# Optimization experiments

Measured on AMD Instinct MI355X. Metric: run time of the kernel, lower is better.

The kernel has to match this reference:

```python
import jax, jax.numpy as jnp
import numpy as np

B, T, E, H, TAG = 32, 1024, 512, 512, 2


def setup_inputs() -> dict:
    key = jax.random.key(0)
    ks = jax.random.split(key, 10)
    s = 1.0 / np.sqrt(H)
    u = lambda k, shape: jax.random.uniform(k, shape, jnp.float32, -s, s)
    xs = jax.random.normal(ks[0], (B, T, E), jnp.float32)
    lengths = jnp.sort(jax.random.randint(ks[1], (B,), 1, T + 1))[::-1]  # pack_padded wants descending
    domains = jnp.ones((B,), jnp.int32)  # single-domain path -> plain model + classification
    return dict(
        xs=xs, lengths=lengths, domains=domains,
        w_ih_f=u(ks[2], (4 * H, E)), w_hh_f=u(ks[3], (4 * H, H)), b_f=u(ks[4], (4 * H,)),
        w_ih_b=u(ks[5], (4 * H, E)), w_hh_b=u(ks[6], (4 * H, H)), b_b=u(ks[7], (4 * H,)),
        w_cls=u(ks[8], (TAG, 2 * H)), b_cls=u(ks[9], (TAG,)),
    )


def _run_lstm(xw, mask, w_hh):
    # xw: [T,B,4H] precomputed x @ W_ih^T + b ; mask: [T,B,1] valid positions
    Hd = w_hh.shape[1]
    Bn = xw.shape[1]

    def step(carry, inp):
        h, c = carry
        xw_t, m = inp
        g = xw_t + h @ w_hh.T                         # [B,4H], torch gate order i,f,g,o
        i, f, gg, o = jnp.split(g, 4, axis=-1)
        c_new = jax.nn.sigmoid(f) * c + jax.nn.sigmoid(i) * jnp.tanh(gg)
        h_new = jax.nn.sigmoid(o) * jnp.tanh(c_new)
        h = jnp.where(m, h_new, h)                    # packed seq: state frozen past length
        c = jnp.where(m, c_new, c)
        return (h, c), h_new * m                      # padded output is zero past length

    init = (jnp.zeros((Bn, Hd), xw.dtype), jnp.zeros((Bn, Hd), xw.dtype))
    _, outs = jax.lax.scan(step, init, (xw, mask))
    return outs  # [T,B,H]


def reference(xs, lengths, domains, w_ih_f, w_hh_f, b_f, w_ih_b, w_hh_b, b_b, w_cls, b_cls):
    Bn, Tn, _ = xs.shape
    t = jnp.arange(Tn)
    mask = (t[:, None] < lengths[None, :])[:, :, None]            # [T,B,1]
    # forward direction
    xw_f = jnp.einsum('bte,ge->tbg', xs, w_ih_f) + b_f
    out_f = _run_lstm(xw_f, mask, w_hh_f)                          # [T,B,H]
    # backward direction: reverse the valid prefix of each sequence
    idx = jnp.where(t[None, :] < lengths[:, None],
                    lengths[:, None] - 1 - t[None, :], t[None, :])  # [B,T]
    xs_rev = jnp.take_along_axis(xs, idx[:, :, None], axis=1)
    xw_b = jnp.einsum('bte,ge->tbg', xs_rev, w_ih_b) + b_b
    out_b_rev = _run_lstm(xw_b, mask, w_hh_b)                      # [T,B,H]
    out_b = jnp.take_along_axis(out_b_rev.transpose(1, 0, 2), idx[:, :, None], axis=1)
    out_b = out_b * mask.transpose(1, 0, 2)                        # zero padded positions
    h = jnp.concatenate([out_f.transpose(1, 0, 2), out_b], axis=-1)  # [B,T,2H]
    logits = h @ w_cls.T + b_cls                                   # [B,T,TAG]
    return jax.nn.softmax(logits, axis=2)
```

## Files before the change

### kernel.cpp

```cpp
#include <hip/hip_runtime.h>
#include <math.h>

#define B_N 32
#define T_N 1024
#define E_N 512
#define H_N 512
#define G4_N 2048

typedef __attribute__((ext_vector_type(8))) short short8;
typedef __attribute__((ext_vector_type(4))) float f32x4;
typedef __attribute__((ext_vector_type(4))) unsigned int uint32x4;
typedef unsigned long long ull;

__device__ __forceinline__ unsigned short f2bfu(float f) {
  unsigned int x = __builtin_bit_cast(unsigned int, f);
  x += 0x7fffu + ((x >> 16) & 1u);
  return (unsigned short)(x >> 16);
}
__device__ __forceinline__ float bfu2f(unsigned short u) {
  return __builtin_bit_cast(float, ((unsigned int)u) << 16);
}
__device__ __forceinline__ float sigmf(float x) { return 1.0f / (1.0f + expf(-x)); }

__device__ __forceinline__ void load64_mall(const unsigned short* p,
                                            uint32x4& a, uint32x4& b,
                                            uint32x4& c, uint32x4& d) {
  asm volatile("global_load_dwordx4 %0, %4, off sc0 sc1\n\t"
               "global_load_dwordx4 %1, %4, off offset:16 sc0 sc1\n\t"
               "global_load_dwordx4 %2, %4, off offset:32 sc0 sc1\n\t"
               "global_load_dwordx4 %3, %4, off offset:48 sc0 sc1\n\t"
               "s_waitcnt vmcnt(0)"
               : "=&v"(a), "=&v"(b), "=&v"(c), "=&v"(d)
               : "v"(p) : "memory");
}
__device__ __forceinline__ void store32_mall(unsigned int* p, unsigned int v) {
  asm volatile("global_store_dword %0, %1, off sc0 sc1" :: "v"(p), "v"(v) : "memory");
}

__global__ __launch_bounds__(256) void xw_gemm_kernel(
    const float* __restrict__ xs, const int* __restrict__ lengths,
    const float* __restrict__ w_ih_f, const float* __restrict__ b_f,
    const float* __restrict__ w_ih_b, const float* __restrict__ b_b,
    unsigned short* __restrict__ xw, int t0, int Tseg)
{
  __shared__ unsigned short As[64][80];
  __shared__ unsigned short Bs[64][80];
  const int g0 = blockIdx.x * 64;
  const int n0 = blockIdx.y * 64;
  const int dir = blockIdx.z;
  const float* __restrict__ W = dir ? w_ih_b : w_ih_f;
  const float* __restrict__ bias = dir ? b_b : b_f;
  const int tid = threadIdx.x;
  const int w = tid >> 6, lane = tid & 63;
  const int wr = w >> 1, wc = w & 1;

  const int sr = tid >> 2;
  const int sq = tid & 3;
  const int nrow = n0 + sr;
  const int bb = nrow & 31;
  const int tt = t0 + (nrow >> 5);
  const int Lb = lengths[bb];
  const int src_t = (dir != 0 && tt < Lb) ? (Lb - 1 - tt) : tt;
  const float* __restrict__ xrow = xs + ((size_t)bb * T_N + src_t) * E_N;
  const float* __restrict__ arow = W + (size_t)(g0 + sr) * E_N;

  f32x4 acc[2][2] = {};

  for (int k0 = 0; k0 < E_N; k0 += 64) {
    float4 av[4], bv[4];
#pragma unroll
    for (int i = 0; i < 4; ++i) {
      av[i] = *(const float4*)&arow[k0 + sq * 16 + i * 4];
      bv[i] = *(const float4*)&xrow[k0 + sq * 16 + i * 4];
    }
    __syncthreads();
#pragma unroll
    for (int i = 0; i < 4; ++i) {
      ushort4 a4, b4;
      a4.x = f2bfu(av[i].x); a4.y = f2bfu(av[i].y); a4.z = f2bfu(av[i].z); a4.w = f2bfu(av[i].w);
      b4.x = f2bfu(bv[i].x); b4.y = f2bfu(bv[i].y); b4.z = f2bfu(bv[i].z); b4.w = f2bfu(bv[i].w);
      *(ushort4*)&As[sr][sq * 16 + i * 4] = a4;
      *(ushort4*)&Bs[sr][sq * 16 + i * 4] = b4;
    }
    __syncthreads();
#pragma unroll
    for (int kk = 0; kk < 2; ++kk) {
      const int ko = kk * 32 + ((lane >> 4) << 3);
      short8 bf0 = *(const short8*)&Bs[wc * 32 + (lane & 15)][ko];
      short8 bf1 = *(const short8*)&Bs[wc * 32 + 16 + (lane & 15)][ko];
      short8 af0 = *(const short8*)&As[wr * 32 + (lane & 15)][ko];
      short8 af1 = *(const short8*)&As[wr * 32 + 16 + (lane & 15)][ko];
      acc[0][0] = __builtin_amdgcn_mfma_f32_16x16x32_bf16(af0, bf0, acc[0][0], 0, 0, 0);
      acc[0][1] = __builtin_amdgcn_mfma_f32_16x16x32_bf16(af0, bf1, acc[0][1], 0, 0, 0);
      acc[1][0] = __builtin_amdgcn_mfma_f32_16x16x32_bf16(af1, bf0, acc[1][0], 0, 0, 0);
      acc[1][1] = __builtin_amdgcn_mfma_f32_16x16x32_bf16(af1, bf1, acc[1][1], 0, 0, 0);
    }
  }

#pragma unroll
  for (int mt = 0; mt < 2; ++mt)
#pragma unroll
    for (int nt = 0; nt < 2; ++nt)
#pragma unroll
      for (int j = 0; j < 4; ++j) {
        const int m = g0 + wr * 32 + mt * 16 + ((lane >> 4) << 2) + j;
        const int n = n0 + wc * 32 + nt * 16 + (lane & 15);
        const int tl = n >> 5, b = n & 31;
        const float v = acc[mt][nt][j] + bias[m];
        xw[(((size_t)dir * Tseg + tl) * G4_N + m) * B_N + b] = f2bfu(v);
      }
}

__global__ __launch_bounds__(512, 1) void rec_kernel(
    const unsigned short* __restrict__ xw,
    const float* __restrict__ w_hh_f, const float* __restrict__ w_hh_b,
    const float* __restrict__ w_cls, const int* __restrict__ lengths,
    unsigned short* __restrict__ hx,
    unsigned int* __restrict__ flg,
    float* __restrict__ c_buf,
    float* __restrict__ lpart,
    int t0, int Tseg)
{
  __shared__ unsigned short Ah[32][520];
  __shared__ float gate_p[8][32][17];
  __shared__ float lp[16][33][2];

  const int tid = threadIdx.x;
  const int wg = blockIdx.x;
  const int dir = wg & 1;
  const int cg = wg >> 1;
  const int colbase = cg * 16;
  const float* __restrict__ w_hh = dir ? w_hh_b : w_hh_f;
  const int w = tid >> 6, lane = tid & 63;
  const int q = w >> 1, kh = w & 1;

  short8 wfrag[8];
  {
    const int grow = q * 512 + colbase + (lane & 15);
    const int kb = (lane >> 4) << 3;
    const float* __restrict__ wr_ = &w_hh[(size_t)grow * H_N + kh * 256];
#pragma unroll
    for (int ks = 0; ks < 8; ++ks) {
      const float4 f0 = *(const float4*)&wr_[ks * 32 + kb];
      const float4 f1 = *(const float4*)&wr_[ks * 32 + kb + 4];
      short8 v;
      v[0] = (short)f2bfu(f0.x); v[1] = (short)f2bfu(f0.y);
      v[2] = (short)f2bfu(f0.z); v[3] = (short)f2bfu(f0.w);
      v[4] = (short)f2bfu(f1.x); v[5] = (short)f2bfu(f1.y);
      v[6] = (short)f2bfu(f1.z); v[7] = (short)f2bfu(f1.w);
      wfrag[ks] = v;
    }
  }

  const int b = tid >> 4;
  const int cl = tid & 15;
  const int col = colbase + cl;
  const int Lb = lengths[b];
  const int Lb_r = lengths[tid & 31];
  float cc = c_buf[((size_t)dir * B_N + b) * H_N + col];
  const float wc0 = w_cls[dir * H_N + col];
  const float wc1 = w_cls[2 * H_N + dir * H_N + col];

  float hh = bfu2f(hx[((size_t)dir * 2 + (t0 & 1)) * 16384 + ((size_t)cg * 32 + b) * 16 + cl]);

  float* __restrict__ lslice = lpart + (size_t)wg * B_N * T_N * 2;
  unsigned int* __restrict__ myflag = flg + dir * 512 + cg * 16;
  unsigned int* __restrict__ pollflag = flg + dir * 512 + (tid >> 4) * 16;

  unsigned short xv[4];
  {
    const unsigned short* __restrict__ xb =
        &xw[((size_t)(dir * Tseg) * G4_N + colbase + cl) * B_N + b];
#pragma unroll
    for (int q2 = 0; q2 < 4; ++q2) xv[q2] = xb[(size_t)q2 * 512 * B_N];
  }

  for (int ts = 0; ts < Tseg; ++ts) {
    const int t = t0 + ts;

    if (ts > 0 && tid < 64) {
      const int br = tid & 31, tau = tid >> 5;
      const int tp = t - 1;
      if (tp < Lb_r) {
        float s = 0.f;
#pragma unroll
        for (int k = 0; k < 16; ++k) s += lp[k][br][tau];
        const int tpos = dir ? (Lb_r - 1 - tp) : tp;
        lslice[((size_t)br * T_N + tpos) * 2 + tau] = s;
      }
    }

    {
      const unsigned int want = (unsigned int)t;
      while (__hip_atomic_load(pollflag, __ATOMIC_RELAXED, __HIP_MEMORY_SCOPE_AGENT) < want) {}
    }
    {
      const unsigned short* hsrc =
          hx + ((size_t)dir * 2 + (t & 1)) * 16384 + (size_t)tid * 32;
      uint32x4 va, vb, vc, vd;
      load64_mall(hsrc, va, vb, vc, vd);
      const int b0 = (tid & 15) * 2, cg16 = (tid >> 4) * 16;
      *(uint32x4*)&Ah[b0][cg16] = va;
      *(uint32x4*)&Ah[b0][cg16 + 8] = vb;
      *(uint32x4*)&Ah[b0 + 1][cg16] = vc;
      *(uint32x4*)&Ah[b0 + 1][cg16 + 8] = vd;
    }
    __syncthreads();

    {
      f32x4 acc0 = {0.f, 0.f, 0.f, 0.f}, acc1 = {0.f, 0.f, 0.f, 0.f};
      const int kb = (lane >> 4) << 3;
#pragma unroll
      for (int ks = 0; ks < 8; ++ks) {
        const int kk = kh * 256 + (ks << 5) + kb;
        short8 a0 = *(const short8*)&Ah[(lane & 15)][kk];
        short8 a1 = *(const short8*)&Ah[16 + (lane & 15)][kk];
        acc0 = __builtin_amdgcn_mfma_f32_16x16x32_bf16(a0, wfrag[ks], acc0, 0, 0, 0);
        acc1 = __builtin_amdgcn_mfma_f32_16x16x32_bf16(a1, wfrag[ks], acc1, 0, 0, 0);
      }
      const int crow = (lane >> 4) << 2;
      const int ccol = lane & 15;
#pragma unroll
      for (int j = 0; j < 4; ++j) {
        gate_p[w][crow + j][ccol] = acc0[j];
        gate_p[w][16 + crow + j][ccol] = acc1[j];
      }
    }
    __syncthreads();

    const bool valid = (t < Lb);
    float hn;
    {
      const float gi = gate_p[0][b][cl] + gate_p[1][b][cl] + bfu2f(xv[0]);
      const float gf = gate_p[2][b][cl] + gate_p[3][b][cl] + bfu2f(xv[1]);
      const float gg = gate_p[4][b][cl] + gate_p[5][b][cl] + bfu2f(xv[2]);
      const float go = gate_p[6][b][cl] + gate_p[7][b][cl] + bfu2f(xv[3]);
      const float cn = sigmf(gf) * cc + sigmf(gi) * tanhf(gg);
      hn = sigmf(go) * tanhf(cn);
      if (valid) { cc = cn; hh = hn; }
    }

    {
      const float hhp = __shfl_xor(hh, 1);
      if ((cl & 1) == 0) {
        const unsigned int pv =
            (unsigned int)f2bfu(hh) | ((unsigned int)f2bfu(hhp) << 16);
        store32_mall((unsigned int*)(hx + ((size_t)dir * 2 + ((t + 1) & 1)) * 16384 +
                                     ((size_t)cg * 32 + b) * 16 + cl),
                     pv);
      }
    }
    lp[cl][b][0] = valid ? hn * wc0 : 0.f;
    lp[cl][b][1] = valid ? hn * wc1 : 0.f;

    __syncthreads();
    if (tid == 0)
      __hip_atomic_store(myflag, (unsigned int)(t + 1),
                         __ATOMIC_RELAXED, __HIP_MEMORY_SCOPE_AGENT);

    if (ts + 1 < Tseg) {
      const unsigned short* __restrict__ xb =
          &xw[((size_t)(dir * Tseg + ts + 1) * G4_N + colbase + cl) * B_N + b];
#pragma unroll
      for (int q2 = 0; q2 < 4; ++q2) xv[q2] = xb[(size_t)q2 * 512 * B_N];
    }
  }

  if (tid < 64) {
    const int br = tid & 31, tau = tid >> 5;
    const int tp = t0 + Tseg - 1;
    if (tp < Lb_r) {
      float s = 0.f;
#pragma unroll
      for (int k = 0; k < 16; ++k) s += lp[k][br][tau];
      const int tpos = dir ? (Lb_r - 1 - tp) : tp;
      lslice[((size_t)br * T_N + tpos) * 2 + tau] = s;
    }
  }

  c_buf[((size_t)dir * B_N + b) * H_N + col] = cc;
}

__global__ void init_kernel(ull* __restrict__ hx64, float* __restrict__ c_buf,
                            unsigned int* __restrict__ flg)
{
  const int i = blockIdx.x * 256 + threadIdx.x;
  if (i < 16384) hx64[i] = 0ull;
  if (i < 2 * B_N * H_N) c_buf[i] = 0.f;
  if (i < 1024) flg[i] = 0u;
}

__global__ void reduce_softmax_kernel(const float* __restrict__ lpart,
                                      const float* __restrict__ b_cls,
                                      float* __restrict__ out)
{
  const int i = blockIdx.x * 256 + threadIdx.x;
  if (i >= B_N * T_N) return;
  float s0 = b_cls[0], s1 = b_cls[1];
  const float* __restrict__ p = lpart + (size_t)i * 2;
#pragma unroll 8
  for (int wg = 0; wg < 64; ++wg) {
    s0 += p[(size_t)wg * B_N * T_N * 2];
    s1 += p[(size_t)wg * B_N * T_N * 2 + 1];
  }
  const float m = fmaxf(s0, s1);
  const float e0 = expf(s0 - m), e1 = expf(s1 - m);
  const float inv = 1.f / (e0 + e1);
  out[2 * i] = e0 * inv;
  out[2 * i + 1] = e1 * inv;
}

extern "C" void kernel_launch(void* const* d_in, const int* in_sizes, int n_in,
                              void* d_out, int out_size, void* d_ws, size_t ws_size,
                              hipStream_t stream)
{
  const float* xs      = (const float*)d_in[0];
  const int*   lengths = (const int*)d_in[1];
  const float* w_ih_f  = (const float*)d_in[3];
  const float* w_hh_f  = (const float*)d_in[4];
  const float* b_f     = (const float*)d_in[5];
  const float* w_ih_b  = (const float*)d_in[6];
  const float* w_hh_b  = (const float*)d_in[7];
  const float* b_b     = (const float*)d_in[8];
  const float* w_cls   = (const float*)d_in[9];
  const float* b_cls   = (const float*)d_in[10];
  float* out = (float*)d_out;

  auto alignup = [](size_t v) { return (v + 255) & ~(size_t)255; };
  const size_t hx_b    = alignup((size_t)2 * 2 * 32 * 32 * 16 * 2);
  const size_t flg_b   = alignup((size_t)1024 * 4);
  const size_t cbuf_b  = alignup((size_t)2 * B_N * H_N * 4);
  const size_t lpart_b = alignup((size_t)64 * B_N * T_N * 2 * 4);
  const size_t fixed = hx_b + flg_b + cbuf_b + lpart_b + 1024;

  int nseg = 1;
  while (nseg < 64) {
    const size_t xwb = alignup((size_t)2 * (T_N / nseg) * G4_N * B_N * 2);
    if (xwb + fixed <= ws_size) break;
    nseg <<= 1;
  }
  const int Tseg = T_N / nseg;
  const size_t xw_b = alignup((size_t)2 * Tseg * G4_N * B_N * 2);

  char* p = (char*)d_ws;
  unsigned short* xw = (unsigned short*)p;  p += xw_b;
  unsigned short* hx = (unsigned short*)p;  p += hx_b;
  unsigned int* flg = (unsigned int*)p;     p += flg_b;
  float* c_buf = (float*)p;                 p += cbuf_b;
  float* lpart = (float*)p;                 p += lpart_b;

  hipMemsetAsync(lpart, 0, lpart_b, stream);
  init_kernel<<<256, 256, 0, stream>>>((ull*)hx, c_buf, flg);

  for (int s = 0; s < nseg; ++s) {
    const int t0 = s * Tseg;
    dim3 g(G4_N / 64, (Tseg * B_N) / 64, 2);
    xw_gemm_kernel<<<g, 256, 0, stream>>>(xs, lengths, w_ih_f, b_f, w_ih_b, b_b, xw, t0, Tseg);
    rec_kernel<<<64, 512, 0, stream>>>(xw, w_hh_f, w_hh_b, w_cls, lengths,
                                       hx, flg, c_buf, lpart, t0, Tseg);
  }

  reduce_softmax_kernel<<<128, 256, 0, stream>>>(lpart, b_cls, out);
}
```

Measured before the change: 4.330 ms.

## Interleave both LSTM directions per workgroup with speculative prefetch of hidden state

```diff
diff --git a/kernel.cpp b/kernel.cpp
--- a/kernel.cpp
+++ b/kernel.cpp
@@ -30,6 +30,16 @@
                "global_load_dwordx4 %2, %4, off offset:32 sc0 sc1\n\t"
                "global_load_dwordx4 %3, %4, off offset:48 sc0 sc1\n\t"
                "s_waitcnt vmcnt(0)"
+               : "=&v"(a), "=&v"(b), "=&v"(c), "=&v"(d)
+               : "v"(p) : "memory");
+}
+__device__ __forceinline__ void load64_mall_nowait(const unsigned short* p,
+                                                   uint32x4& a, uint32x4& b,
+                                                   uint32x4& c, uint32x4& d) {
+  asm volatile("global_load_dwordx4 %0, %4, off sc0 sc1\n\t"
+               "global_load_dwordx4 %1, %4, off offset:16 sc0 sc1\n\t"
+               "global_load_dwordx4 %2, %4, off offset:32 sc0 sc1\n\t"
+               "global_load_dwordx4 %3, %4, off offset:48 sc0 sc1"
                : "=&v"(a), "=&v"(b), "=&v"(c), "=&v"(d)
                : "v"(p) : "memory");
 }
@@ -123,22 +133,26 @@
 {
   __shared__ unsigned short Ah[32][520];
   __shared__ float gate_p[8][32][17];
-  __shared__ float lp[16][33][2];
+  __shared__ float lp[2][16][33][2];
 
   const int tid = threadIdx.x;
-  const int wg = blockIdx.x;
-  const int dir = wg & 1;
-  const int cg = wg >> 1;
+  const int cg = blockIdx.x;
   const int colbase = cg * 16;
-  const float* __restrict__ w_hh = dir ? w_hh_b : w_hh_f;
   const int w = tid >> 6, lane = tid & 63;
   const int q = w >> 1, kh = w & 1;
-
-  short8 wfrag[8];
-  {
+  const int b = tid >> 4;
+  const int cl = tid & 15;
+  const int col = colbase + cl;
+  const int Lb = lengths[b];
+  const int Lb_r = lengths[tid & 31];
+
+  short8 wfrag[2][8];
+#pragma unroll
+  for (int d = 0; d < 2; ++d) {
+    const float* __restrict__ whh = d ? w_hh_b : w_hh_f;
     const int grow = q * 512 + colbase + (lane & 15);
     const int kb = (lane >> 4) << 3;
-    const float* __restrict__ wr_ = &w_hh[(size_t)grow * H_N + kh * 256];
+    const float* __restrict__ wr_ = &whh[(size_t)grow * H_N + kh * 256];
 #pragma unroll
     for (int ks = 0; ks < 8; ++ks) {
       const float4 f0 = *(const float4*)&wr_[ks * 32 + kb];
@@ -148,137 +162,164 @@
       v[2] = (short)f2bfu(f0.z); v[3] = (short)f2bfu(f0.w);
       v[4] = (short)f2bfu(f1.x); v[5] = (short)f2bfu(f1.y);
       v[6] = (short)f2bfu(f1.z); v[7] = (short)f2bfu(f1.w);
-      wfrag[ks] = v;
-    }
-  }
-
-  const int b = tid >> 4;
-  const int cl = tid & 15;
-  const int col = colbase + cl;
-  const int Lb = lengths[b];
-  const int Lb_r = lengths[tid & 31];
-  float cc = c_buf[((size_t)dir * B_N + b) * H_N + col];
-  const float wc0 = w_cls[dir * H_N + col];
-  const float wc1 = w_cls[2 * H_N + dir * H_N + col];
-
-  float hh = bfu2f(hx[((size_t)dir * 2 + (t0 & 1)) * 16384 + ((size_t)cg * 32 + b) * 16 + cl]);
-
-  float* __restrict__ lslice = lpart + (size_t)wg * B_N * T_N * 2;
-  unsigned int* __restrict__ myflag = flg + dir * 512 + cg * 16;
-  unsigned int* __restrict__ pollflag = flg + dir * 512 + (tid >> 4) * 16;
-
-  unsigned short xv[4];
-  {
+      wfrag[d][ks] = v;
+    }
+  }
+
+  float cc[2], hh[2], wc0[2], wc1[2];
+#pragma unroll
+  for (int d = 0; d < 2; ++d) {
+    cc[d] = c_buf[((size_t)d * B_N + b) * H_N + col];
+    hh[d] = bfu2f(hx[((size_t)d * 2 + (t0 & 1)) * 16384 + ((size_t)cg * 32 + b) * 16 + cl]);
+    wc0[d] = w_cls[d * H_N + col];
+    wc1[d] = w_cls[2 * H_N + d * H_N + col];
+  }
+
+  unsigned short xv[2][4];
+#pragma unroll
+  for (int d = 0; d < 2; ++d) {
     const unsigned short* __restrict__ xb =
-        &xw[((size_t)(dir * Tseg) * G4_N + colbase + cl) * B_N + b];
-#pragma unroll
-    for (int q2 = 0; q2 < 4; ++q2) xv[q2] = xb[(size_t)q2 * 512 * B_N];
-  }
+        &xw[((size_t)(d * Tseg) * G4_N + colbase + cl) * B_N + b];
+#pragma unroll
+    for (int q2 = 0; q2 < 4; ++q2) xv[d][q2] = xb[(size_t)q2 * 512 * B_N];
+  }
+
+  uint32x4 sp0, sp1, sp2, sp3;
+  bool spok[2] = {false, false};
+
+  const int myfw = (tid & 15) >> 1;
+  const int b0 = (tid & 15) * 2, cg16 = (tid >> 4) * 16;
 
   for (int ts = 0; ts < Tseg; ++ts) {
     const int t = t0 + ts;
 
-    if (ts > 0 && tid < 64) {
+#pragma unroll
+    for (int d = 0; d < 2; ++d) {
+      const int e = d ^ 1;
+      const int te = t + d;
+
+      if (spok[d]) {
+        asm volatile("s_waitcnt vmcnt(0)" ::: "memory");
+        __builtin_amdgcn_sched_barrier(0);
+        *(uint32x4*)&Ah[b0][cg16] = sp0;
+        *(uint32x4*)&Ah[b0][cg16 + 8] = sp1;
+        *(uint32x4*)&Ah[b0 + 1][cg16] = sp2;
+        *(uint32x4*)&Ah[b0 + 1][cg16 + 8] = sp3;
+      } else {
+        unsigned int* pf = flg + ((size_t)d * 32 + (tid >> 4)) * 8 + myfw;
+        while (__hip_atomic_load(pf, __ATOMIC_RELAXED, __HIP_MEMORY_SCOPE_AGENT) < (unsigned int)t) {}
+        uint32x4 va, vb, vc, vd;
+        load64_mall(hx + ((size_t)d * 2 + (t & 1)) * 16384 + (size_t)tid * 32, va, vb, vc, vd);
+        *(uint32x4*)&Ah[b0][cg16] = va;
+        *(uint32x4*)&Ah[b0][cg16 + 8] = vb;
+        *(uint32x4*)&Ah[b0 + 1][cg16] = vc;
+        *(uint32x4*)&Ah[b0 + 1][cg16 + 8] = vd;
+      }
+      unsigned int fve = __hip_atomic_load(
+          flg + ((size_t)e * 32 + (tid >> 4)) * 8 + myfw,
+          __ATOMIC_RELAXED, __HIP_MEMORY_SCOPE_AGENT);
+
+      __syncthreads();
+
+      if (ts > 0 && tid < 64) {
+        const int br = tid & 31, tau = tid >> 5;
+        const int tp = t - 1;
+        if (tp < Lb_r) {
+          float s = 0.f;
+#pragma unroll
+          for (int k = 0; k < 16; ++k) s += lp[d][k][br][tau];
+          const int tpos = d ? (Lb_r - 1 - tp) : tp;
+          lpart[((size_t)(cg * 2 + d) * B_N + br) * T_N * 2 + (size_t)tpos * 2 + tau] = s;
+        }
+      }
+      unsigned short xvn[4];
+      if (ts + 1 < Tseg) {
+        const unsigned short* __restrict__ xb =
+            &xw[((size_t)(d * Tseg + ts + 1) * G4_N + colbase + cl) * B_N + b];
+#pragma unroll
+        for (int q2 = 0; q2 < 4; ++q2) xvn[q2] = xb[(size_t)q2 * 512 * B_N];
+      }
+
+      {
+        f32x4 acc0 = {0.f, 0.f, 0.f, 0.f}, acc1 = {0.f, 0.f, 0.f, 0.f};
+        const int kb = (lane >> 4) << 3;
+#pragma unroll
+        for (int ks = 0; ks < 8; ++ks) {
+          const int kk = kh * 256 + (ks << 5) + kb;
+          short8 a0 = *(const short8*)&Ah[(lane & 15)][kk];
+          short8 a1 = *(const short8*)&Ah[16 + (lane & 15)][kk];
+          acc0 = __builtin_amdgcn_mfma_f32_16x16x32_bf16(a0, wfrag[d][ks], acc0, 0, 0, 0);
+          acc1 = __builtin_amdgcn_mfma_f32_16x16x32_bf16(a1, wfrag[d][ks], acc1, 0, 0, 0);
+        }
+        const int crow = (lane >> 4) << 2;
+        const int ccol = lane & 15;
+#pragma unroll
+        for (int j = 0; j < 4; ++j) {
+          gate_p[w][crow + j][ccol] = acc0[j];
+          gate_p[w][16 + crow + j][ccol] = acc1[j];
+        }
+      }
+      __syncthreads();
+
+      {
+        const bool in_seg = (d == 0) || (ts + 1 < Tseg);
+        const bool ok = in_seg && __all(fve >= (unsigned int)te);
+        if (ok) {
+          load64_mall_nowait(hx + ((size_t)e * 2 + (te & 1)) * 16384 + (size_t)tid * 32,
+                             sp0, sp1, sp2, sp3);
+        }
+        spok[e] = ok;
+      }
+
+      const bool valid = (t < Lb);
+      float hn;
+      {
+        const float gi = gate_p[0][b][cl] + gate_p[1][b][cl] + bfu2f(xv[d][0]);
+        const float gf = gate_p[2][b][cl] + gate_p[3][b][cl] + bfu2f(xv[d][1]);
+        const float gg = gate_p[4][b][cl] + gate_p[5][b][cl] + bfu2f(xv[d][2]);
+        const float go = gate_p[6][b][cl] + gate_p[7][b][cl] + bfu2f(xv[d][3]);
+        const float cn = sigmf(gf) * cc[d] + sigmf(gi) * tanhf(gg);
+        hn = sigmf(go) * tanhf(cn);
+        if (valid) { cc[d] = cn; hh[d] = hn; }
+      }
+      lp[d][cl][b][0] = valid ? hn * wc0[d] : 0.f;
+      lp[d][cl][b][1] = valid ? hn * wc1[d] : 0.f;
+#pragma unroll
+      for (int q2 = 0; q2 < 4; ++q2) xv[d][q2] = xvn[q2];
+
+      {
+        const float hhp = __shfl_xor(hh[d], 1);
+        if ((cl & 1) == 0) {
+          const unsigned int pv =
+              (unsigned int)f2bfu(hh[d]) | ((unsigned int)f2bfu(hhp) << 16);
+          store32_mall((unsigned int*)(hx + ((size_t)d * 2 + ((t + 1) & 1)) * 16384 +
+                                       ((size_t)cg * 32 + b) * 16 + cl),
+                       pv);
+        }
+      }
+
+      asm volatile("s_waitcnt vmcnt(0)" ::: "memory");
+      __builtin_amdgcn_sched_barrier(0);
+      if (lane == 0)
+        store32_mall(flg + ((size_t)d * 32 + cg) * 8 + w, (unsigned int)(t + 1));
+    }
+  }
+
+#pragma unroll
+  for (int d = 0; d < 2; ++d) {
+    if (tid < 64) {
       const int br = tid & 31, tau = tid >> 5;
-      const int tp = t - 1;
+      const int tp = t0 + Tseg - 1;
       if (tp < Lb_r) {
         float s = 0.f;
 #pragma unroll
-        for (int k = 0; k < 16; ++k) s += lp[k][br][tau];
-        const int tpos = dir ? (Lb_r - 1 - tp) : tp;
-        lslice[((size_t)br * T_N + tpos) * 2 + tau] = s;
-      }
-    }
-
-    {
-      const unsigned int want = (unsigned int)t;
-      while (__hip_atomic_load(pollflag, __ATOMIC_RELAXED, __HIP_MEMORY_SCOPE_AGENT) < want) {}
-    }
-    {
-      const unsigned short* hsrc =
-          hx + ((size_t)dir * 2 + (t & 1)) * 16384 + (size_t)tid * 32;
-      uint32x4 va, vb, vc, vd;
-      load64_mall(hsrc, va, vb, vc, vd);
-      const int b0 = (tid & 15) * 2, cg16 = (tid >> 4) * 16;
-      *(uint32x4*)&Ah[b0][cg16] = va;
-      *(uint32x4*)&Ah[b0][cg16 + 8] = vb;
-      *(uint32x4*)&Ah[b0 + 1][cg16] = vc;
-      *(uint32x4*)&Ah[b0 + 1][cg16 + 8] = vd;
-    }
-    __syncthreads();
-
-    {
-      f32x4 acc0 = {0.f, 0.f, 0.f, 0.f}, acc1 = {0.f, 0.f, 0.f, 0.f};
-      const int kb = (lane >> 4) << 3;
-#pragma unroll
-      for (int ks = 0; ks < 8; ++ks) {
-        const int kk = kh * 256 + (ks << 5) + kb;
-        short8 a0 = *(const short8*)&Ah[(lane & 15)][kk];
-        short8 a1 = *(const short8*)&Ah[16 + (lane & 15)][kk];
-        acc0 = __builtin_amdgcn_mfma_f32_16x16x32_bf16(a0, wfrag[ks], acc0, 0, 0, 0);
-        acc1 = __builtin_amdgcn_mfma_f32_16x16x32_bf16(a1, wfrag[ks], acc1, 0, 0, 0);
-      }
-      const int crow = (lane >> 4) << 2;
-      const int ccol = lane & 15;
-#pragma unroll
-      for (int j = 0; j < 4; ++j) {
-        gate_p[w][crow + j][ccol] = acc0[j];
-        gate_p[w][16 + crow + j][ccol] = acc1[j];
-      }
-    }
-    __syncthreads();
-
-    const bool valid = (t < Lb);
-    float hn;
-    {
-      const float gi = gate_p[0][b][cl] + gate_p[1][b][cl] + bfu2f(xv[0]);
-      const float gf = gate_p[2][b][cl] + gate_p[3][b][cl] + bfu2f(xv[1]);
-      const float gg = gate_p[4][b][cl] + gate_p[5][b][cl] + bfu2f(xv[2]);
-      const float go = gate_p[6][b][cl] + gate_p[7][b][cl] + bfu2f(xv[3]);
-      const float cn = sigmf(gf) * cc + sigmf(gi) * tanhf(gg);
-      hn = sigmf(go) * tanhf(cn);
-      if (valid) { cc = cn; hh = hn; }
-    }
-
-    {
-      const float hhp = __shfl_xor(hh, 1);
-      if ((cl & 1) == 0) {
-        const unsigned int pv =
-            (unsigned int)f2bfu(hh) | ((unsigned int)f2bfu(hhp) << 16);
-        store32_mall((unsigned int*)(hx + ((size_t)dir * 2 + ((t + 1) & 1)) * 16384 +
-                                     ((size_t)cg * 32 + b) * 16 + cl),
-                     pv);
-      }
-    }
-    lp[cl][b][0] = valid ? hn * wc0 : 0.f;
-    lp[cl][b][1] = valid ? hn * wc1 : 0.f;
-
-    __syncthreads();
-    if (tid == 0)
-      __hip_atomic_store(myflag, (unsigned int)(t + 1),
-                         __ATOMIC_RELAXED, __HIP_MEMORY_SCOPE_AGENT);
-
-    if (ts + 1 < Tseg) {
-      const unsigned short* __restrict__ xb =
-          &xw[((size_t)(dir * Tseg + ts + 1) * G4_N + colbase + cl) * B_N + b];
-#pragma unroll
-      for (int q2 = 0; q2 < 4; ++q2) xv[q2] = xb[(size_t)q2 * 512 * B_N];
-    }
-  }
-
-  if (tid < 64) {
-    const int br = tid & 31, tau = tid >> 5;
-    const int tp = t0 + Tseg - 1;
-    if (tp < Lb_r) {
-      float s = 0.f;
-#pragma unroll
-      for (int k = 0; k < 16; ++k) s += lp[k][br][tau];
-      const int tpos = dir ? (Lb_r - 1 - tp) : tp;
-      lslice[((size_t)br * T_N + tpos) * 2 + tau] = s;
-    }
-  }
-
-  c_buf[((size_t)dir * B_N + b) * H_N + col] = cc;
+        for (int k = 0; k < 16; ++k) s += lp[d][k][br][tau];
+        const int tpos = d ? (Lb_r - 1 - tp) : tp;
+        lpart[((size_t)(cg * 2 + d) * B_N + br) * T_N * 2 + (size_t)tpos * 2 + tau] = s;
+      }
+    }
+    c_buf[((size_t)d * B_N + b) * H_N + col] = cc[d];
+  }
 }
 
 __global__ void init_kernel(ull* __restrict__ hx64, float* __restrict__ c_buf,
@@ -287,7 +328,7 @@
   const int i = blockIdx.x * 256 + threadIdx.x;
   if (i < 16384) hx64[i] = 0ull;
   if (i < 2 * B_N * H_N) c_buf[i] = 0.f;
-  if (i < 1024) flg[i] = 0u;
+  if (i < 512) flg[i] = 0u;
 }
 
 __global__ void reduce_softmax_kernel(const float* __restrict__ lpart,
@@ -328,7 +369,7 @@
 
   auto alignup = [](size_t v) { return (v + 255) & ~(size_t)255; };
   const size_t hx_b    = alignup((size_t)2 * 2 * 32 * 32 * 16 * 2);
-  const size_t flg_b   = alignup((size_t)1024 * 4);
+  const size_t flg_b   = alignup((size_t)512 * 4);
   const size_t cbuf_b  = alignup((size_t)2 * B_N * H_N * 4);
   const size_t lpart_b = alignup((size_t)64 * B_N * T_N * 2 * 4);
   const size_t fixed = hx_b + flg_b + cbuf_b + lpart_b + 1024;
@@ -356,7 +397,7 @@
     const int t0 = s * Tseg;
     dim3 g(G4_N / 64, (Tseg * B_N) / 64, 2);
     xw_gemm_kernel<<<g, 256, 0, stream>>>(xs, lengths, w_ih_f, b_f, w_ih_b, b_b, xw, t0, Tseg);
-    rec_kernel<<<64, 512, 0, stream>>>(xw, w_hh_f, w_hh_b, w_cls, lengths,
+    rec_kernel<<<32, 512, 0, stream>>>(xw, w_hh_f, w_hh_b, w_cls, lengths,
                                        hx, flg, c_buf, lpart, t0, Tseg);
   }
 
```

Result: slower. 7.855 ms (+81.4%).

## Use per-wave completion flags and pipelined polling in recurrent LSTM loop

Applied to the files above, without the earlier changes.

```diff
diff --git a/kernel.cpp b/kernel.cpp
--- a/kernel.cpp
+++ b/kernel.cpp
@@ -37,6 +37,23 @@
   asm volatile("global_store_dword %0, %1, off sc0 sc1" :: "v"(p), "v"(v) : "memory");
 }
 
+__device__ __forceinline__ void poll_flag2(const unsigned int* pf, unsigned int want) {
+  unsigned int fa, fb;
+  asm volatile("global_load_dword %0, %2, off sc0 sc1\n\t"
+               "global_load_dword %1, %2, off sc0 sc1"
+               : "=&v"(fa), "=&v"(fb) : "v"(pf) : "memory");
+  for (;;) {
+    asm volatile("s_waitcnt vmcnt(1)" ::: "memory");
+    __builtin_amdgcn_sched_barrier(0);
+    if (fa >= want) break;
+    asm volatile("global_load_dword %0, %1, off sc0 sc1" : "=&v"(fa) : "v"(pf) : "memory");
+    asm volatile("s_waitcnt vmcnt(1)" ::: "memory");
+    __builtin_amdgcn_sched_barrier(0);
+    if (fb >= want) break;
+    asm volatile("global_load_dword %0, %1, off sc0 sc1" : "=&v"(fb) : "v"(pf) : "memory");
+  }
+}
+
 __global__ __launch_bounds__(256) void xw_gemm_kernel(
     const float* __restrict__ xs, const int* __restrict__ lengths,
     const float* __restrict__ w_ih_f, const float* __restrict__ b_f,
@@ -164,8 +181,9 @@
   float hh = bfu2f(hx[((size_t)dir * 2 + (t0 & 1)) * 16384 + ((size_t)cg * 32 + b) * 16 + cl]);
 
   float* __restrict__ lslice = lpart + (size_t)wg * B_N * T_N * 2;
-  unsigned int* __restrict__ myflag = flg + dir * 512 + cg * 16;
-  unsigned int* __restrict__ pollflag = flg + dir * 512 + (tid >> 4) * 16;
+  unsigned int* __restrict__ myflag = flg + ((size_t)dir * 32 + cg) * 8 + w;
+  const unsigned int* __restrict__ pollflag =
+      flg + ((size_t)dir * 32 + (tid >> 4)) * 8 + ((tid & 15) >> 1);
 
   unsigned short xv[4];
   {
@@ -175,8 +193,22 @@
     for (int q2 = 0; q2 < 4; ++q2) xv[q2] = xb[(size_t)q2 * 512 * B_N];
   }
 
+  const int b0 = (tid & 15) * 2, cg16 = (tid >> 4) * 16;
+
   for (int ts = 0; ts < Tseg; ++ts) {
     const int t = t0 + ts;
+
+    poll_flag2(pollflag, (unsigned int)t);
+    {
+      uint32x4 va, vb, vc, vd;
+      load64_mall(hx + ((size_t)dir * 2 + (t & 1)) * 16384 + (size_t)tid * 32,
+                  va, vb, vc, vd);
+      *(uint32x4*)&Ah[b0][cg16] = va;
+      *(uint32x4*)&Ah[b0][cg16 + 8] = vb;
+      *(uint32x4*)&Ah[b0 + 1][cg16] = vc;
+      *(uint32x4*)&Ah[b0 + 1][cg16 + 8] = vd;
+    }
+    __syncthreads();
 
     if (ts > 0 && tid < 64) {
       const int br = tid & 31, tau = tid >> 5;
@@ -189,23 +221,6 @@
         lslice[((size_t)br * T_N + tpos) * 2 + tau] = s;
       }
     }
-
-    {
-      const unsigned int want = (unsigned int)t;
-      while (__hip_atomic_load(pollflag, __ATOMIC_RELAXED, __HIP_MEMORY_SCOPE_AGENT) < want) {}
-    }
-    {
-      const unsigned short* hsrc =
-          hx + ((size_t)dir * 2 + (t & 1)) * 16384 + (size_t)tid * 32;
-      uint32x4 va, vb, vc, vd;
-      load64_mall(hsrc, va, vb, vc, vd);
-      const int b0 = (tid & 15) * 2, cg16 = (tid >> 4) * 16;
-      *(uint32x4*)&Ah[b0][cg16] = va;
-      *(uint32x4*)&Ah[b0][cg16 + 8] = vb;
-      *(uint32x4*)&Ah[b0 + 1][cg16] = vc;
-      *(uint32x4*)&Ah[b0 + 1][cg16 + 8] = vd;
-    }
-    __syncthreads();
 
     {
       f32x4 acc0 = {0.f, 0.f, 0.f, 0.f}, acc1 = {0.f, 0.f, 0.f, 0.f};
@@ -253,10 +268,10 @@
     lp[cl][b][0] = valid ? hn * wc0 : 0.f;
     lp[cl][b][1] = valid ? hn * wc1 : 0.f;
 
-    __syncthreads();
-    if (tid == 0)
-      __hip_atomic_store(myflag, (unsigned int)(t + 1),
-                         __ATOMIC_RELAXED, __HIP_MEMORY_SCOPE_AGENT);
+    asm volatile("s_waitcnt vmcnt(0)" ::: "memory");
+    __builtin_amdgcn_sched_barrier(0);
+    if (lane == 0)
+      store32_mall(myflag, (unsigned int)(t + 1));
 
     if (ts + 1 < Tseg) {
       const unsigned short* __restrict__ xb =
```

New measurement: 4.453 ms. +2.9%, slower.

## Overlap next-segment input GEMM with recurrence in a fused kernel; trim to max length

Applied to the files above, without the earlier changes.

```diff
diff --git a/kernel.cpp b/kernel.cpp
--- a/kernel.cpp
+++ b/kernel.cpp
@@ -111,28 +111,103 @@
       }
 }
 
-__global__ __launch_bounds__(512, 1) void rec_kernel(
-    const unsigned short* __restrict__ xw,
+__global__ __launch_bounds__(512, 1) void fused_kernel(
+    const float* __restrict__ xs, const int* __restrict__ lengths,
+    const float* __restrict__ w_ih_f, const float* __restrict__ b_f,
+    const float* __restrict__ w_ih_b, const float* __restrict__ b_b,
     const float* __restrict__ w_hh_f, const float* __restrict__ w_hh_b,
-    const float* __restrict__ w_cls, const int* __restrict__ lengths,
+    const float* __restrict__ w_cls,
+    const unsigned short* __restrict__ xw_cur,
+    unsigned short* __restrict__ xw_nxt,
     unsigned short* __restrict__ hx,
     unsigned int* __restrict__ flg,
     float* __restrict__ c_buf,
     float* __restrict__ lpart,
-    int t0, int Tseg)
+    int t0, int Tseg, int t0n)
 {
-  __shared__ unsigned short Ah[32][520];
-  __shared__ float gate_p[8][32][17];
-  __shared__ float lp[16][33][2];
-
+  __shared__ alignas(16) unsigned char smem[86016];
   const int tid = threadIdx.x;
+  const int w = tid >> 6, lane = tid & 63;
+  const int Lmax = lengths[0];
+
+  if (blockIdx.x >= 64) {
+    if (t0n >= T_N || t0n >= Lmax) return;
+    unsigned short* As = (unsigned short*)smem;
+    unsigned short* Bs = (unsigned short*)(smem + 10240);
+    const int g = blockIdx.x - 64;
+    const int wr = w >> 2, wc = w & 3;
+    const int sr = tid >> 3, sq = tid & 7;
+    const int ntau = 2 * 32 * (Tseg >> 1);
+
+    for (int tau = g; tau < ntau; tau += 192) {
+      const int gtile = tau & 31;
+      const int rest = tau >> 5;
+      const int dir = rest & 1;
+      const int ntile = rest >> 1;
+      const int tt0 = t0n + ntile * 2;
+      if (tt0 >= Lmax) continue;
+      const int g0 = gtile * 64;
+      const float* __restrict__ W = dir ? w_ih_b : w_ih_f;
+      const float* __restrict__ bias = dir ? b_b : b_f;
+      const int bb = sr & 31;
+      const int tt = tt0 + (sr >> 5);
+      const int Lb2 = lengths[bb];
+      const int src_t = (dir != 0 && tt < Lb2) ? (Lb2 - 1 - tt) : tt;
+      const float* __restrict__ xrow = xs + ((size_t)bb * T_N + src_t) * E_N;
+      const float* __restrict__ arow = W + (size_t)(g0 + sr) * E_N;
+      f32x4 accm0 = {0.f, 0.f, 0.f, 0.f}, accm1 = {0.f, 0.f, 0.f, 0.f};
+
+      for (int k0 = 0; k0 < E_N; k0 += 64) {
+        const float4 av0 = *(const float4*)&arow[k0 + sq * 8];
+        const float4 av1 = *(const float4*)&arow[k0 + sq * 8 + 4];
+        const float4 bv0 = *(const float4*)&xrow[k0 + sq * 8];
+        const float4 bv1 = *(const float4*)&xrow[k0 + sq * 8 + 4];
+        __syncthreads();
+        ushort4 u;
+        u.x = f2bfu(av0.x); u.y = f2bfu(av0.y); u.z = f2bfu(av0.z); u.w = f2bfu(av0.w);
+        *(ushort4*)&As[sr * 80 + sq * 8] = u;
+        u.x = f2bfu(av1.x); u.y = f2bfu(av1.y); u.z = f2bfu(av1.z); u.w = f2bfu(av1.w);
+        *(ushort4*)&As[sr * 80 + sq * 8 + 4] = u;
+        u.x = f2bfu(bv0.x); u.y = f2bfu(bv0.y); u.z = f2bfu(bv0.z); u.w = f2bfu(bv0.w);
+        *(ushort4*)&Bs[sr * 80 + sq * 8] = u;
+        u.x = f2bfu(bv1.x); u.y = f2bfu(bv1.y); u.z = f2bfu(bv1.z); u.w = f2bfu(bv1.w);
+        *(ushort4*)&Bs[sr * 80 + sq * 8 + 4] = u;
+        __syncthreads();
+#pragma unroll
+        for (int kk = 0; kk < 2; ++kk) {
+          const int ko = kk * 32 + ((lane >> 4) << 3);
+          short8 bf  = *(const short8*)&Bs[(wc * 16 + (lane & 15)) * 80 + ko];
+          short8 af0 = *(const short8*)&As[(wr * 32 + (lane & 15)) * 80 + ko];
+          short8 af1 = *(const short8*)&As[(wr * 32 + 16 + (lane & 15)) * 80 + ko];
+          accm0 = __builtin_amdgcn_mfma_f32_16x16x32_bf16(af0, bf, accm0, 0, 0, 0);
+          accm1 = __builtin_amdgcn_mfma_f32_16x16x32_bf16(af1, bf, accm1, 0, 0, 0);
+        }
+      }
+#pragma unroll
+      for (int mt = 0; mt < 2; ++mt)
+#pragma unroll
+        for (int j = 0; j < 4; ++j) {
+          const int m = g0 + wr * 32 + mt * 16 + ((lane >> 4) << 2) + j;
+          const int n = ntile * 64 + wc * 16 + (lane & 15);
+          const int tl = n >> 5, b = n & 31;
+          const float v = (mt ? accm1[j] : accm0[j]) + bias[m];
+          xw_nxt[(((size_t)dir * Tseg + tl) * G4_N + m) * B_N + b] = f2bfu(v);
+        }
+    }
+    return;
+  }
+
+  unsigned short (*Ah)[520] = (unsigned short (*)[520])smem;
+  float (*gate_p)[32][17] = (float (*)[32][17])(smem + 33280);
+  float (*lp)[33][2] = (float (*)[33][2])(smem + 50688);
+
   const int wg = blockIdx.x;
   const int dir = wg & 1;
   const int cg = wg >> 1;
   const int colbase = cg * 16;
   const float* __restrict__ w_hh = dir ? w_hh_b : w_hh_f;
-  const int w = tid >> 6, lane = tid & 63;
   const int q = w >> 1, kh = w & 1;
+  const int Tloc = min(Tseg, max(0, Lmax - t0));
 
   short8 wfrag[8];
   {
@@ -168,14 +243,16 @@
   unsigned int* __restrict__ pollflag = flg + dir * 512 + (tid >> 4) * 16;
 
   unsigned short xv[4];
-  {
+  if (Tloc > 0) {
     const unsigned short* __restrict__ xb =
-        &xw[((size_t)(dir * Tseg) * G4_N + colbase + cl) * B_N + b];
+        &xw_cur[((size_t)(dir * Tseg) * G4_N + colbase + cl) * B_N + b];
 #pragma unroll
     for (int q2 = 0; q2 < 4; ++q2) xv[q2] = xb[(size_t)q2 * 512 * B_N];
   }
 
-  for (int ts = 0; ts < Tseg; ++ts) {
+  const int b0 = (tid & 15) * 2, cg16 = (tid >> 4) * 16;
+
+  for (int ts = 0; ts < Tloc; ++ts) {
     const int t = t0 + ts;
 
     if (ts > 0 && tid < 64) {
@@ -195,11 +272,9 @@
       while (__hip_atomic_load(pollflag, __ATOMIC_RELAXED, __HIP_MEMORY_SCOPE_AGENT) < want) {}
     }
     {
-      const unsigned short* hsrc =
-          hx + ((size_t)dir * 2 + (t & 1)) * 16384 + (size_t)tid * 32;
       uint32x4 va, vb, vc, vd;
-      load64_mall(hsrc, va, vb, vc, vd);
-      const int b0 = (tid & 15) * 2, cg16 = (tid >> 4) * 16;
+      load64_mall(hx + ((size_t)dir * 2 + (t & 1)) * 16384 + (size_t)tid * 32,
+                  va, vb, vc, vd);
       *(uint32x4*)&Ah[b0][cg16] = va;
       *(uint32x4*)&Ah[b0][cg16 + 8] = vb;
       *(uint32x4*)&Ah[b0 + 1][cg16] = vc;
@@ -258,17 +333,17 @@
       __hip_atomic_store(myflag, (unsigned int)(t + 1),
                          __ATOMIC_RELAXED, __HIP_MEMORY_SCOPE_AGENT);
 
-    if (ts + 1 < Tseg) {
+    if (ts + 1 < Tloc) {
       const unsigned short* __restrict__ xb =
-          &xw[((size_t)(dir * Tseg + ts + 1) * G4_N + colbase + cl) * B_N + b];
+          &xw_cur[((size_t)(dir * Tseg + ts + 1) * G4_N + colbase + cl) * B_N + b];
 #pragma unroll
       for (int q2 = 0; q2 < 4; ++q2) xv[q2] = xb[(size_t)q2 * 512 * B_N];
     }
   }
 
-  if (tid < 64) {
+  if (Tloc > 0 && tid < 64) {
     const int br = tid & 31, tau = tid >> 5;
-    const int tp = t0 + Tseg - 1;
+    const int tp = t0 + Tloc - 1;
     if (tp < Lb_r) {
       float s = 0.f;
 #pragma unroll
@@ -336,28 +411,36 @@
   int nseg = 1;
   while (nseg < 64) {
     const size_t xwb = alignup((size_t)2 * (T_N / nseg) * G4_N * B_N * 2);
-    if (xwb + fixed <= ws_size) break;
+    if (2 * xwb + fixed <= ws_size) break;
     nseg <<= 1;
   }
   const int Tseg = T_N / nseg;
   const size_t xw_b = alignup((size_t)2 * Tseg * G4_N * B_N * 2);
 
   char* p = (char*)d_ws;
-  unsigned short* xw = (unsigned short*)p;  p += xw_b;
+  unsigned short* xw0 = (unsigned short*)p; p += xw_b;
+  unsigned short* xw1 = (unsigned short*)p; p += xw_b;
   unsigned short* hx = (unsigned short*)p;  p += hx_b;
   unsigned int* flg = (unsigned int*)p;     p += flg_b;
   float* c_buf = (float*)p;                 p += cbuf_b;
   float* lpart = (float*)p;                 p += lpart_b;
+  unsigned short* bufs[2] = {xw0, xw1};
 
   hipMemsetAsync(lpart, 0, lpart_b, stream);
   init_kernel<<<256, 256, 0, stream>>>((ull*)hx, c_buf, flg);
 
+  {
+    dim3 g(G4_N / 64, (Tseg * B_N) / 64, 2);
+    xw_gemm_kernel<<<g, 256, 0, stream>>>(xs, lengths, w_ih_f, b_f, w_ih_b, b_b,
+                                          bufs[0], 0, Tseg);
+  }
+
   for (int s = 0; s < nseg; ++s) {
     const int t0 = s * Tseg;
-    dim3 g(G4_N / 64, (Tseg * B_N) / 64, 2);
-    xw_gemm_kernel<<<g, 256, 0, stream>>>(xs, lengths, w_ih_f, b_f, w_ih_b, b_b, xw, t0, Tseg);
-    rec_kernel<<<64, 512, 0, stream>>>(xw, w_hh_f, w_hh_b, w_cls, lengths,
-                                       hx, flg, c_buf, lpart, t0, Tseg);
+    fused_kernel<<<256, 512, 0, stream>>>(
+        xs, lengths, w_ih_f, b_f, w_ih_b, b_b, w_hh_f, w_hh_b, w_cls,
+        bufs[s & 1], bufs[(s + 1) & 1], hx, flg, c_buf, lpart,
+        t0, Tseg, t0 + Tseg);
   }
 
   reduce_softmax_kernel<<<128, 256, 0, stream>>>(lpart, b_cls, out);
```

New measurement: 3.752 ms. 13.3% less time.
